# Kernel optimization log

Measured on AMD Instinct MI355X. Metric: run time of the kernel, lower is better.

Reference implementation:

```python
import jax, jax.numpy as jnp
import numpy as np

B, T, V, D, H, C = 256, 512, 400000, 50, 50, 5  # batch, seq, vocab, emb_dim, lstm_hidden, classes


def setup_inputs() -> dict:
    key = jax.random.key(0)
    ks = jax.random.split(key, 9)
    x = jax.random.randint(ks[0], (B, T), 0, V)
    lengths = jax.random.randint(ks[1], (B,), 1, T + 1)
    bows = jnp.zeros((B, 1), dtype=jnp.float32)  # unused by the model
    emb_table = jax.random.normal(ks[2], (V, D), dtype=jnp.float32) * 0.1
    s = 1.0 / np.sqrt(H)
    W_ih = jax.random.uniform(ks[3], (4 * H, D), minval=-s, maxval=s, dtype=jnp.float32)
    W_hh = jax.random.uniform(ks[4], (4 * H, H), minval=-s, maxval=s, dtype=jnp.float32)
    b_ih = jax.random.uniform(ks[5], (4 * H,), minval=-s, maxval=s, dtype=jnp.float32)
    b_hh = jax.random.uniform(ks[6], (4 * H,), minval=-s, maxval=s, dtype=jnp.float32)
    sl = 1.0 / np.sqrt(3 * H)
    W_lin = jax.random.uniform(ks[7], (C, 3 * H), minval=-sl, maxval=sl, dtype=jnp.float32)
    b_lin = jax.random.uniform(ks[8], (C,), minval=-sl, maxval=sl, dtype=jnp.float32)
    return {"x": x, "lengths": lengths, "bows": bows, "emb_table": emb_table,
            "W_ih": W_ih, "W_hh": W_hh, "b_ih": b_ih, "b_hh": b_hh,
            "W_lin": W_lin, "b_lin": b_lin}


def _lstm(emb, W_ih, W_hh, b_ih, b_hh):
    # emb: [B,T,D] -> h_all: [B,T,H]; PyTorch gate order i,f,g,o
    xp = jnp.einsum('btd,gd->btg', emb, W_ih) + b_ih + b_hh  # [B,T,4H]
    xp_t = jnp.swapaxes(xp, 0, 1)  # [T,B,4H]
    h0 = jnp.zeros((emb.shape[0], W_hh.shape[1]), emb.dtype)
    c0 = jnp.zeros_like(h0)

    def step(carry, xt):
        h, c = carry
        g = xt + h @ W_hh.T
        i, f, gg, o = jnp.split(g, 4, axis=-1)
        i, f, o = jax.nn.sigmoid(i), jax.nn.sigmoid(f), jax.nn.sigmoid(o)
        c = f * c + i * jnp.tanh(gg)
        h = o * jnp.tanh(c)
        return (h, c), h

    _, h_all = jax.lax.scan(step, (h0, c0), xp_t)
    return jnp.swapaxes(h_all, 0, 1)  # [B,T,H]


def reference(x, lengths, bows, emb_table, W_ih, W_hh, b_ih, b_hh, W_lin, b_lin):
    emb = emb_table[x]                              # [B,T,D]
    h_all = _lstm(emb, W_ih, W_hh, b_ih, b_hh)      # [B,T,H]
    idx = jnp.minimum(lengths, h_all.shape[1]) - 1  # last valid timestep
    last = jnp.take_along_axis(h_all, idx[:, None, None], axis=1)[:, 0, :]  # [B,H]
    # faithful to original: sum over full padded seq / length, max over full padded seq
    mean = jnp.sum(emb, axis=1) / lengths[:, None].astype(emb.dtype)        # [B,D]
    mx = jnp.max(emb, axis=1)                                               # [B,D]
    rep = jnp.concatenate([last, mean, mx], axis=1)                          # [B,3H]
    return rep @ W_lin.T + b_lin
```

## Files before the change

kernel.cpp:

```cpp
#include <hip/hip_runtime.h>
#include <cmath>

#define NB 256
#define NT 512
#define ND 50
#define NH 50
#define NC 5

typedef float f32x4 __attribute__((ext_vector_type(4)));
typedef float f32x2 __attribute__((ext_vector_type(2)));

__device__ __forceinline__ float rcpf(float x) { return __builtin_amdgcn_rcpf(x); }
__device__ __forceinline__ float rdl(float v, int l) {
    return __int_as_float(__builtin_amdgcn_readlane(__float_as_int(v), l));
}
__device__ __forceinline__ void gload4(f32x4& d, const float* p) {
    asm volatile("global_load_dwordx4 %0, %1, off" : "=v"(d) : "v"(p));
}

#define FENCE_BAR                                             \
    asm volatile("s_waitcnt lgkmcnt(0)" ::: "memory");        \
    __builtin_amdgcn_s_barrier();                             \
    asm volatile("" ::: "memory");

__global__ __launch_bounds__(256)
void k0_prep(const float* __restrict__ W_hh, const float* __restrict__ W_ih,
             float* __restrict__ wsWih, float* __restrict__ wsWhh)
{
    int idx = blockIdx.x * 256 + threadIdx.x;
    if (idx < 200 * 52) {
        int d = idx / 52, c = idx - (idx / 52) * 52;
        wsWih[idx] = (c < ND) ? W_ih[d * ND + c] : 0.f;
    } else if (idx < 2 * 200 * 52) {
        int j = idx - 200 * 52;
        int d = j / 52, c = j - (j / 52) * 52;
        wsWhh[j] = (c < NH) ? W_hh[d * NH + c] : 0.f;
    }
}

#define DECLROW(P) f32x4 P##_0{},P##_1{},P##_2{},P##_3{},P##_4{},P##_5{},P##_6{},P##_7{}, \
                         P##_8{},P##_9{},P##_10{},P##_11{},P##_12{};
#define LOADROW(P,B) { const float* b_=(B); \
    gload4(P##_0,b_+0);  gload4(P##_1,b_+4);  gload4(P##_2,b_+8);  gload4(P##_3,b_+12); \
    gload4(P##_4,b_+16); gload4(P##_5,b_+20); gload4(P##_6,b_+24); gload4(P##_7,b_+28); \
    gload4(P##_8,b_+32); gload4(P##_9,b_+36); gload4(P##_10,b_+40); gload4(P##_11,b_+44); \
    gload4(P##_12,b_+48); }

#define FMA2(H,W,A) __builtin_elementwise_fma((H),(W),(A))
#define KP(J) { f32x2 eA = ep[2*(J)], eB = ep[2*(J)+1];                       \
    A01 = FMA2(eA, w##J.xy, A01); A23 = FMA2(eB, w##J.zw, A23); }

__global__ __launch_bounds__(256)
void k1_xproj(const int* __restrict__ x, const int* __restrict__ lengths,
              const float* __restrict__ emb_table,
              const float* __restrict__ wsWih, const float* __restrict__ b_ih,
              const float* __restrict__ b_hh,
              float* __restrict__ xp, int t0, int t1, int tiles, int tcAlloc)
{
    const int b    = blockIdx.x / tiles;
    const int tile = blockIdx.x % tiles;
    const int rt0  = t0 + tile * 64;
    if (rt0 >= t1) return;
    if (rt0 >= lengths[b]) return;
    const int nrows = min(64, t1 - rt0);

    const int tid = threadIdx.x;
    const int* xrow = x + (size_t)b * NT + rt0;

    float bsum = 0.f;
    const float* wrow = wsWih + tid * 52;
    f32x4 w0{},w1{},w2{},w3{},w4{},w5{},w6{},w7{},w8{},w9{},w10{},w11{},w12{};
    gload4(w0,wrow+0); gload4(w1,wrow+4); gload4(w2,wrow+8); gload4(w3,wrow+12);
    gload4(w4,wrow+16); gload4(w5,wrow+20); gload4(w6,wrow+24); gload4(w7,wrow+28);
    gload4(w8,wrow+32); gload4(w9,wrow+36); gload4(w10,wrow+40); gload4(w11,wrow+44);
    gload4(w12,wrow+48);
    if (tid < 200) bsum = b_ih[tid] + b_hh[tid];
    asm volatile("s_waitcnt vmcnt(0)" ::: "memory");
    __builtin_amdgcn_sched_barrier(0);

    if (tid < 200) {
        const int wr = 4 * (tid % NH) + (tid / NH);
        float* xpb = xp + ((size_t)b * tcAlloc + (rt0 - t0)) * 200 + wr;
        for (int row = 0; row < nrows; ++row) {
            int xr = __builtin_amdgcn_readfirstlane(xrow[row]);
            const f32x2* ep = (const f32x2*)(emb_table + (size_t)xr * ND);
            f32x2 A01 = {bsum, 0.f}, A23 = {0.f, 0.f};
            KP(0) KP(1) KP(2) KP(3) KP(4) KP(5) KP(6) KP(7) KP(8) KP(9) KP(10) KP(11)
            A01 = FMA2(ep[24], w12.xy, A01);
            xpb[(size_t)row * 200] = (A01.x + A01.y) + (A23.x + A23.y);
        }
    }
}

#define CDOT1(SEED,OUT) { f32x2 A01 = {(SEED), 0.f}, A23 = {0.f, 0.f};        \
    A01=FMA2(hp0 ,CW_0.xy ,A01); A23=FMA2(hp1 ,CW_0.zw ,A23);                 \
    A01=FMA2(hp2 ,CW_1.xy ,A01); A23=FMA2(hp3 ,CW_1.zw ,A23);                 \
    A01=FMA2(hp4 ,CW_2.xy ,A01); A23=FMA2(hp5 ,CW_2.zw ,A23);                 \
    A01=FMA2(hp6 ,CW_3.xy ,A01); A23=FMA2(hp7 ,CW_3.zw ,A23);                 \
    A01=FMA2(hp8 ,CW_4.xy ,A01); A23=FMA2(hp9 ,CW_4.zw ,A23);                 \
    A01=FMA2(hp10,CW_5.xy ,A01); A23=FMA2(hp11,CW_5.zw ,A23);                 \
    A01=FMA2(hp12,CW_6.xy ,A01); A23=FMA2(hp13,CW_6.zw ,A23);                 \
    A01=FMA2(hp14,CW_7.xy ,A01); A23=FMA2(hp15,CW_7.zw ,A23);                 \
    A01=FMA2(hp16,CW_8.xy ,A01); A23=FMA2(hp17,CW_8.zw ,A23);                 \
    A01=FMA2(hp18,CW_9.xy ,A01); A23=FMA2(hp19,CW_9.zw ,A23);                 \
    A01=FMA2(hp20,CW_10.xy,A01); A23=FMA2(hp21,CW_10.zw,A23);                 \
    A01=FMA2(hp22,CW_11.xy,A01); A23=FMA2(hp23,CW_11.zw,A23);                 \
    A23=FMA2(hp24,CW_12.xy,A23);                                              \
    OUT = (A01.x + A01.y) + (A23.x + A23.y); }

#define SSTEP(XQ, S) {                                                        \
    f32x2 hp0 ={rdl(hv,0 ),rdl(hv,1 )}, hp1 ={rdl(hv,2 ),rdl(hv,3 )};         \
    f32x2 hp2 ={rdl(hv,4 ),rdl(hv,5 )}, hp3 ={rdl(hv,6 ),rdl(hv,7 )};         \
    f32x2 hp4 ={rdl(hv,8 ),rdl(hv,9 )}, hp5 ={rdl(hv,10),rdl(hv,11)};         \
    f32x2 hp6 ={rdl(hv,12),rdl(hv,13)}, hp7 ={rdl(hv,14),rdl(hv,15)};         \
    f32x2 hp8 ={rdl(hv,16),rdl(hv,17)}, hp9 ={rdl(hv,18),rdl(hv,19)};         \
    f32x2 hp10={rdl(hv,20),rdl(hv,21)}, hp11={rdl(hv,22),rdl(hv,23)};         \
    f32x2 hp12={rdl(hv,24),rdl(hv,25)}, hp13={rdl(hv,26),rdl(hv,27)};         \
    f32x2 hp14={rdl(hv,28),rdl(hv,29)}, hp15={rdl(hv,30),rdl(hv,31)};         \
    f32x2 hp16={rdl(hv,32),rdl(hv,33)}, hp17={rdl(hv,34),rdl(hv,35)};         \
    f32x2 hp18={rdl(hv,36),rdl(hv,37)}, hp19={rdl(hv,38),rdl(hv,39)};         \
    f32x2 hp20={rdl(hv,40),rdl(hv,41)}, hp21={rdl(hv,42),rdl(hv,43)};         \
    f32x2 hp22={rdl(hv,44),rdl(hv,45)}, hp23={rdl(hv,46),rdl(hv,47)};         \
    f32x2 hp24={rdl(hv,48),rdl(hv,49)};                                       \
    float gg;                                                                 \
    CDOT1(XQ, gg)                                                             \
    { int sn_ = (S) + 4; if (sn_ > nsteps - 1) sn_ = nsteps - 1;              \
      XQ = xpb[(size_t)sn_ * 200]; }                                          \
    float act = fmaf(rcpf(1.f + __expf(-sce * gg)), sce, ade);                \
    abuf[(S) & 1][wid][kln] = act;                                            \
    FENCE_BAR                                                                 \
    float i_ = abuf[(S) & 1][0][kln];                                         \
    float f_ = abuf[(S) & 1][1][kln];                                         \
    float gt = abuf[(S) & 1][2][kln];                                         \
    float o_ = abuf[(S) & 1][3][kln];                                         \
    cst = fmaf(f_, cst, i_ * gt);                                             \
    float th = fmaf(rcpf(1.f + __expf(-2.f * cst)), 2.f, -1.f);               \
    hv = o_ * th;                                                             \
    hkeep = (t0 + (S) == lastidx) ? hv : hkeep;                               \
}

__global__ __launch_bounds__(256)
__attribute__((amdgpu_waves_per_eu(1, 1)))
void k2_scan(const int* __restrict__ lengths, const float* __restrict__ wsWhh,
             const float* __restrict__ xp,
             float* __restrict__ stH, float* __restrict__ stC, float* __restrict__ lastH,
             int t0, int t1, int tcAlloc)
{
    const int b   = blockIdx.x, tid = threadIdx.x;
    const int wid = tid >> 6;
    const int kln = tid & 63;
    const int kc  = (kln < NH) ? kln : NH - 1;

    __shared__ __align__(16) float abuf[2][4][64];

    const int lastidx = min(lengths[b], NT) - 1;
    const int nsteps  = t1 - t0;

    float hv  = (t0 == 0) ? 0.f : stH[b * NH + kc];
    float cst = (t0 == 0) ? 0.f : stC[b * NH + kc];

    DECLROW(CW)
    LOADROW(CW, wsWhh + ((size_t)wid * NH + kc) * 52)
    asm volatile("s_waitcnt vmcnt(0)" ::: "memory");
    __builtin_amdgcn_sched_barrier(0);

    const float sce = (wid == 2) ? 2.f : 1.f;
    const float ade = (wid == 2) ? -1.f : 0.f;

    const float* xpb = xp + (size_t)b * tcAlloc * 200 + 4 * kc + wid;
    float xq0 = xpb[0];
    float xq1 = xpb[200];
    float xq2 = xpb[400];
    float xq3 = xpb[600];
    float hkeep = 0.f;

    for (int s4 = 0; s4 < nsteps; s4 += 4) {
        SSTEP(xq0, s4 + 0)
        SSTEP(xq1, s4 + 1)
        SSTEP(xq2, s4 + 2)
        SSTEP(xq3, s4 + 3)
    }

    if (wid == 0 && kln < NH) {
        stH[b * NH + kln] = hv;
        stC[b * NH + kln] = cst;
        if (lastidx >= t0 && lastidx < t1) lastH[b * NH + kln] = hkeep;
    }
}

__global__ __launch_bounds__(256)
void k3_final(const int* __restrict__ x, const int* __restrict__ lengths,
              const float* __restrict__ emb_table,
              const float* __restrict__ W_lin, const float* __restrict__ b_lin,
              const float* __restrict__ lastH, float* __restrict__ out)
{
    const int b = blockIdx.x, tid = threadIdx.x;
    __shared__ int xv[NT];
    __shared__ float ps[5][52], pm[5][52];
    __shared__ float rep[160];

    for (int i = tid; i < NT; i += 256) xv[i] = x[(size_t)b * NT + i];
    __syncthreads();
    const int g = tid / ND, d = tid - g * ND;
    if (tid < 250) {
        float s = 0.f, m = -INFINITY;
        #pragma unroll 4
        for (int t = g; t < NT; t += 5) {
            float e = emb_table[(size_t)xv[t] * ND + d];
            s += e; m = fmaxf(m, e);
        }
        ps[g][d] = s; pm[g][d] = m;
    }
    __syncthreads();
    if (tid < NH) {
        float s = ps[0][tid] + ps[1][tid] + ps[2][tid] + ps[3][tid] + ps[4][tid];
        float m = fmaxf(fmaxf(fmaxf(pm[0][tid], pm[1][tid]), fmaxf(pm[2][tid], pm[3][tid])), pm[4][tid]);
        rep[tid]          = lastH[b * NH + tid];
        rep[NH + tid]     = s / (float)lengths[b];
        rep[2 * NH + tid] = m;
    }
    __syncthreads();
    if (tid < NC) {
        float acc = b_lin[tid];
        #pragma unroll 5
        for (int j = 0; j < 3 * NH; ++j)
            acc = fmaf(rep[j], W_lin[tid * 3 * NH + j], acc);
        out[(size_t)b * NC + tid] = acc;
    }
}

extern "C" void kernel_launch(void* const* d_in, const int* in_sizes, int n_in,
                              void* d_out, int out_size, void* d_ws, size_t ws_size,
                              hipStream_t stream) {
    const int*   x     = (const int*)d_in[0];
    const int*   len   = (const int*)d_in[1];
    const float* emb   = (const float*)d_in[3];
    const float* W_ih  = (const float*)d_in[4];
    const float* W_hh  = (const float*)d_in[5];
    const float* b_ih  = (const float*)d_in[6];
    const float* b_hh  = (const float*)d_in[7];
    const float* W_lin = (const float*)d_in[8];
    const float* b_lin = (const float*)d_in[9];
    float* outp = (float*)d_out;

    float* stH   = (float*)d_ws;
    float* stC   = stH + NB * NH;
    float* lastH = stC + NB * NH;
    float* wsWih = (float*)((char*)d_ws + 160 * 1024);
    float* wsWhh = wsWih + 200 * 52;
    const size_t xpOff = 256 * 1024;
    float* xp = (float*)((char*)d_ws + xpOff);

    size_t avail = (ws_size > xpOff + 8192) ? ws_size - xpOff - 8192 : 0;
    int tc = (int)(avail / ((size_t)NB * 200 * sizeof(float)));
    tc &= ~3;
    if (tc > NT) tc = NT;
    if (tc < 4)  tc = 4;

    hipLaunchKernelGGL(k0_prep, dim3(82), dim3(256), 0, stream, W_hh, W_ih, wsWih, wsWhh);

    for (int t0 = 0; t0 < NT; t0 += tc) {
        const int t1 = min(NT, t0 + tc);
        const int tiles = (t1 - t0 + 63) / 64;
        hipLaunchKernelGGL(k1_xproj, dim3(NB * tiles), dim3(256), 0, stream,
                           x, len, emb, wsWih, b_ih, b_hh, xp, t0, t1, tiles, tc);
        hipLaunchKernelGGL(k2_scan, dim3(NB), dim3(256), 0, stream,
                           len, wsWhh, xp, stH, stC, lastH, t0, t1, tc);
    }
    hipLaunchKernelGGL(k3_final, dim3(NB), dim3(256), 0, stream,
                       x, len, emb, W_lin, b_lin, lastH, outp);
}
```

Baseline: 254.0 us.

## Fuse final pooling/linear into scan kernel and unroll xproj two rows

The final kernel that does the mean/max pooling and the linear layer is merged into the tail of the last scan launch, which removes one kernel launch and the reload of lastH. Separately, the input-projection kernel now handles two timesteps per iteration and prefetches the next token indices, giving more independent gather loads and FMAs in flight. The fused tail adds LDS use to the scan kernel and runs pooling serially after the recurrence. The two-row loop assumes an even row count per tile; with an odd count it would read one index past the end.

```diff
diff --git a/kernel.cpp b/kernel.cpp
--- a/kernel.cpp
+++ b/kernel.cpp
@@ -47,8 +47,9 @@
     gload4(P##_12,b_+48); }
 
 #define FMA2(H,W,A) __builtin_elementwise_fma((H),(W),(A))
-#define KP(J) { f32x2 eA = ep[2*(J)], eB = ep[2*(J)+1];                       \
-    A01 = FMA2(eA, w##J.xy, A01); A23 = FMA2(eB, w##J.zw, A23); }
+#define KP2(J) { f32x2 a_=e0[2*(J)], b_=e0[2*(J)+1], c_=e1[2*(J)], d_=e1[2*(J)+1]; \
+    A01=FMA2(a_,w##J.xy,A01); A23=FMA2(b_,w##J.zw,A23);                            \
+    B01=FMA2(c_,w##J.xy,B01); B23=FMA2(d_,w##J.zw,B23); }
 
 __global__ __launch_bounds__(256)
 void k1_xproj(const int* __restrict__ x, const int* __restrict__ lengths,
@@ -81,13 +82,23 @@
     if (tid < 200) {
         const int wr = 4 * (tid % NH) + (tid / NH);
         float* xpb = xp + ((size_t)b * tcAlloc + (rt0 - t0)) * 200 + wr;
-        for (int row = 0; row < nrows; ++row) {
-            int xr = __builtin_amdgcn_readfirstlane(xrow[row]);
-            const f32x2* ep = (const f32x2*)(emb_table + (size_t)xr * ND);
+        int xr0 = __builtin_amdgcn_readfirstlane(xrow[0]);
+        int xr1 = __builtin_amdgcn_readfirstlane(xrow[1]);
+        for (int row = 0; row < nrows; row += 2) {
+            const f32x2* e0 = (const f32x2*)(emb_table + (size_t)xr0 * ND);
+            const f32x2* e1 = (const f32x2*)(emb_table + (size_t)xr1 * ND);
+            const int nr = (row + 2 < nrows) ? row + 2 : 0;
+            int nx0 = __builtin_amdgcn_readfirstlane(xrow[nr]);
+            int nx1 = __builtin_amdgcn_readfirstlane(xrow[nr + 1]);
             f32x2 A01 = {bsum, 0.f}, A23 = {0.f, 0.f};
-            KP(0) KP(1) KP(2) KP(3) KP(4) KP(5) KP(6) KP(7) KP(8) KP(9) KP(10) KP(11)
-            A01 = FMA2(ep[24], w12.xy, A01);
-            xpb[(size_t)row * 200] = (A01.x + A01.y) + (A23.x + A23.y);
+            f32x2 B01 = {bsum, 0.f}, B23 = {0.f, 0.f};
+            KP2(0) KP2(1) KP2(2) KP2(3) KP2(4) KP2(5)
+            KP2(6) KP2(7) KP2(8) KP2(9) KP2(10) KP2(11)
+            A01 = FMA2(e0[24], w12.xy, A01);
+            B01 = FMA2(e1[24], w12.xy, B01);
+            xpb[(size_t)row * 200]       = (A01.x + A01.y) + (A23.x + A23.y);
+            xpb[(size_t)(row + 1) * 200] = (B01.x + B01.y) + (B23.x + B23.y);
+            xr0 = nx0; xr1 = nx1;
         }
     }
 }
@@ -141,10 +152,12 @@
 
 __global__ __launch_bounds__(256)
 __attribute__((amdgpu_waves_per_eu(1, 1)))
-void k2_scan(const int* __restrict__ lengths, const float* __restrict__ wsWhh,
-             const float* __restrict__ xp,
+void k2_scan(const int* __restrict__ x, const int* __restrict__ lengths,
+             const float* __restrict__ emb_table,
+             const float* __restrict__ wsWhh, const float* __restrict__ xp,
+             const float* __restrict__ W_lin, const float* __restrict__ b_lin,
              float* __restrict__ stH, float* __restrict__ stC, float* __restrict__ lastH,
-             int t0, int t1, int tcAlloc)
+             float* __restrict__ out, int t0, int t1, int tcAlloc)
 {
     const int b   = blockIdx.x, tid = threadIdx.x;
     const int wid = tid >> 6;
@@ -152,6 +165,9 @@
     const int kc  = (kln < NH) ? kln : NH - 1;
 
     __shared__ __align__(16) float abuf[2][4][64];
+    __shared__ int xv[NT];
+    __shared__ float ps[5][52], pm[5][52];
+    __shared__ float rep[160];
 
     const int lastidx = min(lengths[b], NT) - 1;
     const int nsteps  = t1 - t0;
@@ -186,46 +202,37 @@
         stC[b * NH + kln] = cst;
         if (lastidx >= t0 && lastidx < t1) lastH[b * NH + kln] = hkeep;
     }
-}
-
-__global__ __launch_bounds__(256)
-void k3_final(const int* __restrict__ x, const int* __restrict__ lengths,
-              const float* __restrict__ emb_table,
-              const float* __restrict__ W_lin, const float* __restrict__ b_lin,
-              const float* __restrict__ lastH, float* __restrict__ out)
-{
-    const int b = blockIdx.x, tid = threadIdx.x;
-    __shared__ int xv[NT];
-    __shared__ float ps[5][52], pm[5][52];
-    __shared__ float rep[160];
-
-    for (int i = tid; i < NT; i += 256) xv[i] = x[(size_t)b * NT + i];
-    __syncthreads();
-    const int g = tid / ND, d = tid - g * ND;
-    if (tid < 250) {
-        float s = 0.f, m = -INFINITY;
-        #pragma unroll 4
-        for (int t = g; t < NT; t += 5) {
-            float e = emb_table[(size_t)xv[t] * ND + d];
-            s += e; m = fmaxf(m, e);
-        }
-        ps[g][d] = s; pm[g][d] = m;
-    }
-    __syncthreads();
-    if (tid < NH) {
-        float s = ps[0][tid] + ps[1][tid] + ps[2][tid] + ps[3][tid] + ps[4][tid];
-        float m = fmaxf(fmaxf(fmaxf(pm[0][tid], pm[1][tid]), fmaxf(pm[2][tid], pm[3][tid])), pm[4][tid]);
-        rep[tid]          = lastH[b * NH + tid];
-        rep[NH + tid]     = s / (float)lengths[b];
-        rep[2 * NH + tid] = m;
-    }
-    __syncthreads();
-    if (tid < NC) {
-        float acc = b_lin[tid];
-        #pragma unroll 5
-        for (int j = 0; j < 3 * NH; ++j)
-            acc = fmaf(rep[j], W_lin[tid * 3 * NH + j], acc);
-        out[(size_t)b * NC + tid] = acc;
+
+    if (t1 == NT) {
+        for (int i = tid; i < NT; i += 256) xv[i] = x[(size_t)b * NT + i];
+        __syncthreads();
+        const int g5 = tid / ND, d5 = tid - g5 * ND;
+        if (tid < 250) {
+            float s = 0.f, m = -INFINITY;
+            #pragma unroll 4
+            for (int t = g5; t < NT; t += 5) {
+                float e = emb_table[(size_t)xv[t] * ND + d5];
+                s += e; m = fmaxf(m, e);
+            }
+            ps[g5][d5] = s; pm[g5][d5] = m;
+        }
+        __syncthreads();
+        if (tid < NH) {
+            float s = ps[0][tid] + ps[1][tid] + ps[2][tid] + ps[3][tid] + ps[4][tid];
+            float m = fmaxf(fmaxf(fmaxf(pm[0][tid], pm[1][tid]),
+                                  fmaxf(pm[2][tid], pm[3][tid])), pm[4][tid]);
+            rep[tid]          = (lastidx >= t0) ? hkeep : lastH[b * NH + tid];
+            rep[NH + tid]     = s / (float)lengths[b];
+            rep[2 * NH + tid] = m;
+        }
+        __syncthreads();
+        if (tid < NC) {
+            float acc = b_lin[tid];
+            #pragma unroll 5
+            for (int j = 0; j < 3 * NH; ++j)
+                acc = fmaf(rep[j], W_lin[tid * 3 * NH + j], acc);
+            out[(size_t)b * NC + tid] = acc;
+        }
     }
 }
 
@@ -265,8 +272,7 @@
         hipLaunchKernelGGL(k1_xproj, dim3(NB * tiles), dim3(256), 0, stream,
                            x, len, emb, wsWih, b_ih, b_hh, xp, t0, t1, tiles, tc);
         hipLaunchKernelGGL(k2_scan, dim3(NB), dim3(256), 0, stream,
-                           len, wsWhh, xp, stH, stC, lastH, t0, t1, tc);
-    }
-    hipLaunchKernelGGL(k3_final, dim3(NB), dim3(256), 0, stream,
-                       x, len, emb, W_lin, b_lin, lastH, outp);
-}
+                           x, len, emb, wsWhh, xp, W_lin, b_lin,
+                           stH, stC, lastH, outp, t0, t1, tc);
+    }
+}
```

Result: faster. 249.0 us (-2.0%).
